# Kernel optimization log

Measured on AMD Instinct MI355X. Metric: run time of the kernel, lower is better.

Reference implementation:

```python
import jax, jax.numpy as jnp
import numpy as np

U, T, Q, K, H = 2048, 200, 4096, 16, 256
STD_THETA = 1.0
LMDA_THETA = 1.0 / STD_THETA**2


def setup_inputs() -> dict:
    key = jax.random.key(0)
    ks = jax.random.split(key, 10)
    q_id = jax.random.randint(ks[0], (U, T), 0, Q)
    kmap = jax.random.bernoulli(ks[1], 0.25, (Q, K))
    mask = jnp.ones((U, T), dtype=bool)
    resp = jnp.round(jax.random.uniform(ks[2], (U, T))).astype(jnp.float32)
    diff_mu = jax.random.normal(ks[3], (Q,), jnp.float32) * 0.5
    disc_mu = jax.random.normal(ks[4], (Q,), jnp.float32) * 0.5
    W1 = jax.random.normal(ks[5], (3, H), jnp.float32) * 0.3
    b1 = jnp.zeros((H,), jnp.float32)
    W2 = jax.random.normal(ks[6], (H, H), jnp.float32) * (1.0 / np.sqrt(H))
    b2 = jnp.zeros((H,), jnp.float32)
    W3 = jax.random.normal(ks[7], (H, 2), jnp.float32) * (1.0 / np.sqrt(H))
    b3 = jnp.zeros((2,), jnp.float32)
    return dict(mask=mask, q_id=q_id, kmap=kmap, resp=resp,
                diff_mu=diff_mu, disc_mu=disc_mu,
                W1=W1, b1=b1, W2=W2, b2=b2, W3=W3, b3=b3)


def _gelu(x):
    return jax.nn.gelu(x, approximate=False)  # torch nn.GELU default (erf)


def reference(mask, q_id, kmap, resp, diff_mu, disc_mu, W1, b1, W2, b2, W3, b3):
    # --- per-trial potentials (MLP input is identical across the KC axis) ---
    td = diff_mu[q_id]                       # (U,T)  diff gather
    ts = disc_mu[q_id]                       # (U,T)  disc gather
    inp = jnp.stack([td, ts, resp], axis=-1)  # (U,T,3)
    h = _gelu(inp @ W1 + b1)
    h = _gelu(h @ W2 + b2)
    poten = _gelu(h @ W3 + b3)               # (U,T,2)
    mu = poten[..., 0]                       # (U,T)
    logvar = jnp.maximum(poten[..., 1], 1e-8)
    lmda = jnp.exp(-logvar)                  # (U,T)

    m = jnp.moveaxis(kmap[q_id], 1, 0)       # (T,U,K) trial KC mask
    mu_T = mu.T                              # (T,U)
    lmda_T = lmda.T                          # (T,U)
    zUK = jnp.zeros((mu.shape[0], m.shape[-1]), mu.dtype)  # (U,K)

    # --- backward (Kalman-style) alpha/beta recursion; unmasked slots carry ---
    def bwd(carry, xs):
        alpha, beta = carry                  # (U,K) each
        l, mu_, msk = xs                     # (U,), (U,), (U,K)
        l = l[:, None]
        mu_ = mu_[:, None]
        a_new = (l + alpha * LMDA_THETA) / (LMDA_THETA + l + alpha * LMDA_THETA)
        b_new = (l * mu_ + a_new * l * beta) / (l + a_new * l)
        alpha2 = jnp.where(msk, a_new, alpha)
        beta2 = jnp.where(msk, b_new, beta)
        return (alpha2, beta2), alpha2

    _, alphas = jax.lax.scan(bwd, (zUK, zUK), (lmda_T, mu_T, m), reverse=True)
    # alpha_next[t] = alpha_{t+1} (zero past the end)
    alpha_next = jnp.concatenate([alphas[1:], zUK[None]], axis=0)  # (T,U,K)

    # --- forward posterior-mean ability update (deterministic mean path) ---
    def fwd(ability, xs):
        l, mu_, msk, a_nxt = xs
        l = l[:, None]
        mu_ = mu_[:, None]
        b_nxt = a_nxt  # replicates original: beta_next = alpha_lst[t+1]
        mu_tilde = (LMDA_THETA * ability + mu_ * l + a_nxt * LMDA_THETA * b_nxt) \
                   / (LMDA_THETA + l + a_nxt * LMDA_THETA)
        ab = jnp.where(msk, mu_tilde, ability)  # masked scatter / carry-through
        return ab, ab

    _, ab_tk = jax.lax.scan(fwd, zUK, (lmda_T, mu_T, m, alpha_next))  # (T,U,K)

    mf = m.astype(mu.dtype)
    trial_ability = ((ab_tk * mf).sum(-1) / jnp.maximum(mf.sum(-1), 1e-8)).T  # (U,T)
    return trial_ability
```

## Files before the change

kernel.cpp:

```cpp
#include <hip/hip_runtime.h>
#include <hip/hip_bf16.h>
#include <stdint.h>

#define U_DIM 2048
#define T_DIM 200
#define Q_DIM 4096
#define K_DIM 16
#define H_DIM 256
#define N_ROWS (Q_DIM * 2)

typedef float f4 __attribute__((ext_vector_type(4)));
typedef float f2 __attribute__((ext_vector_type(2)));

__device__ __forceinline__ float gelu_f(float x) {
    return 0.5f * x * (1.0f + erff(x * 0.70710678118654752440f));
}

__global__ __launch_bounds__(256) void pack_kmap_kernel(
    const uint8_t* __restrict__ kmap, uint32_t* __restrict__ mask_tab)
{
    __shared__ uint32_t sflag;
    int tid = threadIdx.x;
    if (tid < 64) {
        const uint32_t* kw = (const uint32_t*)kmap;
        uint32_t any = 0;
        #pragma unroll
        for (int i = 0; i < 16; ++i) any |= (kw[tid + 64 * i] > 1u) ? 1u : 0u;
        uint64_t b = __ballot(any != 0);
        if (tid == 0) sflag = (b != 0) ? 1u : 0u;
    }
    __syncthreads();
    int q = blockIdx.x * 256 + tid;
    uint32_t m = 0;
    if (sflag) {
        const uint32_t* p = (const uint32_t*)(kmap + (size_t)q * K_DIM);
        #pragma unroll
        for (int w = 0; w < 4; ++w) {
            uint32_t v = p[w];
            #pragma unroll
            for (int b = 0; b < 4; ++b)
                m |= (((v >> (8 * b)) & 0xffu) ? 1u : 0u) << (4 * w + b);
        }
    } else {
        const int* ki = (const int*)kmap + (size_t)q * K_DIM;
        #pragma unroll
        for (int k = 0; k < K_DIM; ++k)
            m |= (ki[k] ? 1u : 0u) << k;
    }
    mask_tab[q] = m;
}

__global__ __launch_bounds__(256) void mlp_table_kernel(
    const float* __restrict__ diff_mu, const float* __restrict__ disc_mu,
    const float* __restrict__ W1, const float* __restrict__ b1,
    const float* __restrict__ W2, const float* __restrict__ b2,
    const float* __restrict__ W3, const float* __restrict__ b3,
    float* __restrict__ mu_tab, float* __restrict__ lmda_tab)
{
    __shared__ float h1t[H_DIM][8];
    __shared__ float red[4][8][H_DIM];
    int tid  = threadIdx.x;
    int lane = tid & 63;
    int w    = tid >> 6;
    int row0 = blockIdx.x * 8;

    {
        int i = 64 * w + lane;
        float w1a = W1[0 * H_DIM + i], w1b = W1[1 * H_DIM + i],
              w1c = W1[2 * H_DIM + i], bi = b1[i];
        float hv[8];
        #pragma unroll
        for (int g = 0; g < 8; ++g) {
            int row = row0 + g;
            float td = diff_mu[row >> 1];
            float ts = disc_mu[row >> 1];
            float rr = (float)(row & 1);
            hv[g] = gelu_f(td * w1a + ts * w1b + rr * w1c + bi);
        }
        *(f4*)&h1t[i][0] = (f4){hv[0], hv[1], hv[2], hv[3]};
        *(f4*)&h1t[i][4] = (f4){hv[4], hv[5], hv[6], hv[7]};
    }
    __syncthreads();

    float acc[8][4];
    #pragma unroll
    for (int g = 0; g < 8; ++g) { acc[g][0] = acc[g][1] = acc[g][2] = acc[g][3] = 0.0f; }
    #pragma unroll 4
    for (int s = 0; s < 64; ++s) {
        int i = 64 * w + s;
        f4 wv = *(const f4*)&W2[i * H_DIM + 4 * lane];
        f4 hA = *(const f4*)&h1t[i][0];
        f4 hB = *(const f4*)&h1t[i][4];
        #pragma unroll
        for (int c = 0; c < 4; ++c) {
            acc[0][c] += hA[0] * wv[c];
            acc[1][c] += hA[1] * wv[c];
            acc[2][c] += hA[2] * wv[c];
            acc[3][c] += hA[3] * wv[c];
            acc[4][c] += hB[0] * wv[c];
            acc[5][c] += hB[1] * wv[c];
            acc[6][c] += hB[2] * wv[c];
            acc[7][c] += hB[3] * wv[c];
        }
    }
    #pragma unroll
    for (int g = 0; g < 8; ++g)
        *(f4*)&red[w][g][4 * lane] = (f4){acc[g][0], acc[g][1], acc[g][2], acc[g][3]};
    __syncthreads();

    if (tid < 128) {
        int w2 = tid >> 6;
        int l  = tid & 63;
        f4 bb2  = *(const f4*)&b2[4 * l];
        f4 w3lo = *(const f4*)&W3[8 * l];
        f4 w3hi = *(const f4*)&W3[8 * l + 4];
        float p0[4], p1[4];
        #pragma unroll
        for (int gg = 0; gg < 4; ++gg) {
            int g = 4 * w2 + gg;
            f4 s = bb2;
            #pragma unroll
            for (int ww = 0; ww < 4; ++ww) {
                f4 r = *(const f4*)&red[ww][g][4 * l];
                s[0] += r[0]; s[1] += r[1]; s[2] += r[2]; s[3] += r[3];
            }
            float h0 = gelu_f(s[0]), h1v = gelu_f(s[1]),
                  h2v = gelu_f(s[2]), h3v = gelu_f(s[3]);
            p0[gg] = h0 * w3lo[0] + h1v * w3lo[2] + h2v * w3hi[0] + h3v * w3hi[2];
            p1[gg] = h0 * w3lo[1] + h1v * w3lo[3] + h2v * w3hi[1] + h3v * w3hi[3];
        }
        #pragma unroll
        for (int gg = 0; gg < 4; ++gg) {
            #pragma unroll
            for (int off = 1; off < 64; off <<= 1) {
                p0[gg] += __shfl_xor(p0[gg], off);
                p1[gg] += __shfl_xor(p1[gg], off);
            }
        }
        if (l == 0) {
            float bb30 = b3[0], bb31 = b3[1];
            #pragma unroll
            for (int gg = 0; gg < 4; ++gg) {
                int row = row0 + 4 * w2 + gg;
                float mu = gelu_f(p0[gg] + bb30);
                float lv = gelu_f(p1[gg] + bb31);
                mu_tab[row]   = mu;
                lmda_tab[row] = expf(-fmaxf(lv, 1e-8f));
            }
        }
    }
}

__global__ __launch_bounds__(64) void scan_fused_kernel(
    const int* __restrict__ q_id, const float* __restrict__ resp,
    const float* __restrict__ mu_tab, const float* __restrict__ lmda_tab,
    const uint32_t* __restrict__ mask_tab, float* __restrict__ out)
{
    __shared__ float a_lds[64][201];
    __shared__ f2 la_lds[4][T_DIM];
    __shared__ uint16_t mk_lds[4][T_DIM];
    int tid = threadIdx.x;
    int u0 = blockIdx.x * 4;

    int   qv[13];
    float rv[13];
    #pragma unroll
    for (int p = 0; p < 13; ++p) {
        int idx = tid + 64 * p;
        if (idx < 4 * T_DIM) {
            int ul = idx / T_DIM, t = idx - ul * T_DIM;
            int g = (u0 + ul) * T_DIM + t;
            qv[p] = q_id[g];
            rv[p] = resp[g];
        }
    }
    #pragma unroll
    for (int p = 0; p < 13; ++p) {
        int idx = tid + 64 * p;
        if (idx < 4 * T_DIM) {
            int ul = idx / T_DIM, t = idx - ul * T_DIM;
            int ix = 2 * qv[p] + (rv[p] != 0.0f ? 1 : 0);
            float l  = lmda_tab[ix];
            float mu = mu_tab[ix];
            la_lds[ul][t] = (f2){1.0f + l, mu * l};
            mk_lds[ul][t] = (uint16_t)mask_tab[qv[p]];
        }
    }
    __syncthreads();

    int ul = tid >> 4, k = tid & 15;
    float* ap = a_lds[tid];
    const f2* la = la_lds[ul];
    const uint16_t* mk = mk_lds[ul];

    float alpha = 0.0f;
    float L1s0 = la[196][0], L1s1 = la[197][0], L1s2 = la[198][0], L1s3 = la[199][0];
    uint32_t ms0 = mk[196], ms1 = mk[197], ms2 = mk[198], ms3 = mk[199];
    for (int tb = 196; tb >= 0; tb -= 4) {
        int p3 = (tb >= 1) ? tb - 1 : 0;
        int p2 = (tb >= 2) ? tb - 2 : 0;
        int p1 = (tb >= 3) ? tb - 3 : 0;
        int p0 = (tb >= 4) ? tb - 4 : 0;
        { float L1 = L1s3; uint32_t m = ms3; L1s3 = la[p3][0]; ms3 = mk[p3];
          ap[tb + 3] = alpha;
          float an = 1.0f - __builtin_amdgcn_rcpf(L1 + alpha);
          alpha = ((m >> k) & 1) ? an : alpha; }
        { float L1 = L1s2; uint32_t m = ms2; L1s2 = la[p2][0]; ms2 = mk[p2];
          ap[tb + 2] = alpha;
          float an = 1.0f - __builtin_amdgcn_rcpf(L1 + alpha);
          alpha = ((m >> k) & 1) ? an : alpha; }
        { float L1 = L1s1; uint32_t m = ms1; L1s1 = la[p1][0]; ms1 = mk[p1];
          ap[tb + 1] = alpha;
          float an = 1.0f - __builtin_amdgcn_rcpf(L1 + alpha);
          alpha = ((m >> k) & 1) ? an : alpha; }
        { float L1 = L1s0; uint32_t m = ms0; L1s0 = la[p0][0]; ms0 = mk[p0];
          ap[tb + 0] = alpha;
          float an = 1.0f - __builtin_amdgcn_rcpf(L1 + alpha);
          alpha = ((m >> k) & 1) ? an : alpha; }
    }

    float ability = 0.0f;
    f2 lv0 = la[0], lv1 = la[1], lv2 = la[2], lv3 = la[3];
    uint32_t n0 = mk[0], n1 = mk[1], n2 = mk[2], n3 = mk[3];
    float av0 = ap[0], av1 = ap[1], av2 = ap[2], av3 = ap[3];
    for (int tb = 0; tb < 200; tb += 4) {
        int p0 = (tb + 4 < 200) ? tb + 4 : 199;
        int p1 = (tb + 5 < 200) ? tb + 5 : 199;
        int p2 = (tb + 6 < 200) ? tb + 6 : 199;
        int p3 = (tb + 7 < 200) ? tb + 7 : 199;
        { f2 v = lv0; uint32_t m = n0; float a = av0;
          lv0 = la[p0]; n0 = mk[p0]; av0 = ap[p0];
          float r = __builtin_amdgcn_rcpf(v[0] + a);
          float c1 = v[1] + a * a;
          float mt = (ability + c1) * r;
          bool msk = (m >> k) & 1;
          ability = msk ? mt : ability;
          ap[tb + 0] = msk ? ability : 0.0f; }
        { f2 v = lv1; uint32_t m = n1; float a = av1;
          lv1 = la[p1]; n1 = mk[p1]; av1 = ap[p1];
          float r = __builtin_amdgcn_rcpf(v[0] + a);
          float c1 = v[1] + a * a;
          float mt = (ability + c1) * r;
          bool msk = (m >> k) & 1;
          ability = msk ? mt : ability;
          ap[tb + 1] = msk ? ability : 0.0f; }
        { f2 v = lv2; uint32_t m = n2; float a = av2;
          lv2 = la[p2]; n2 = mk[p2]; av2 = ap[p2];
          float r = __builtin_amdgcn_rcpf(v[0] + a);
          float c1 = v[1] + a * a;
          float mt = (ability + c1) * r;
          bool msk = (m >> k) & 1;
          ability = msk ? mt : ability;
          ap[tb + 2] = msk ? ability : 0.0f; }
        { f2 v = lv3; uint32_t m = n3; float a = av3;
          lv3 = la[p3]; n3 = mk[p3]; av3 = ap[p3];
          float r = __builtin_amdgcn_rcpf(v[0] + a);
          float c1 = v[1] + a * a;
          float mt = (ability + c1) * r;
          bool msk = (m >> k) & 1;
          ability = msk ? mt : ability;
          ap[tb + 3] = msk ? ability : 0.0f; }
    }
    __syncthreads();

    #pragma unroll
    for (int p = 0; p < 13; ++p) {
        int idx = tid + 64 * p;
        if (idx < 4 * T_DIM) {
            int uo = idx / T_DIM, t = idx - uo * T_DIM;
            float s = 0.0f;
            #pragma unroll
            for (int kk = 0; kk < 16; ++kk) s += a_lds[uo * 16 + kk][t];
            float c = (float)__popc((unsigned)(mk_lds[uo][t] & 0xffffu));
            out[(u0 + uo) * T_DIM + t] = s * __builtin_amdgcn_rcpf(fmaxf(c, 1e-8f));
        }
    }
}

extern "C" void kernel_launch(void* const* d_in, const int* in_sizes, int n_in,
                              void* d_out, int out_size, void* d_ws, size_t ws_size,
                              hipStream_t stream) {
    const int*     q_id    = (const int*)d_in[1];
    const uint8_t* kmap    = (const uint8_t*)d_in[2];
    const float*   resp    = (const float*)d_in[3];
    const float*   diff_mu = (const float*)d_in[4];
    const float*   disc_mu = (const float*)d_in[5];
    const float*   W1      = (const float*)d_in[6];
    const float*   b1      = (const float*)d_in[7];
    const float*   W2      = (const float*)d_in[8];
    const float*   b2      = (const float*)d_in[9];
    const float*   W3      = (const float*)d_in[10];
    const float*   b3      = (const float*)d_in[11];
    float* out = (float*)d_out;

    char* w = (char*)d_ws;
    float* mu_tab      = (float*)w;      w += (size_t)N_ROWS * 4;
    float* lmda_tab    = (float*)w;      w += (size_t)N_ROWS * 4;
    uint32_t* mask_tab = (uint32_t*)w;   w += (size_t)Q_DIM * 4;

    hipLaunchKernelGGL(pack_kmap_kernel, dim3(Q_DIM / 256), dim3(256), 0, stream,
                       kmap, mask_tab);
    hipLaunchKernelGGL(mlp_table_kernel, dim3(N_ROWS / 8), dim3(256), 0, stream,
                       diff_mu, disc_mu, W1, b1, W2, b2, W3, b3, mu_tab, lmda_tab);
    hipLaunchKernelGGL(scan_fused_kernel, dim3(U_DIM / 4), dim3(64), 0, stream,
                       q_id, resp, mu_tab, lmda_tab, mask_tab, out);
}
```

Baseline: 121.9 us.

## Fuse kmap packing into MLP table kernel and double rows per block

Merges the kmap bit-packing kernel into the MLP table kernel, so the first 16 blocks also build the mask table, which removes one kernel launch. Each block now handles 16 table rows instead of 8, halving the grid and reusing each W2 load across twice as many rows. The cross-wave reduction runs in two phases over a reused shared buffer. This raises register pressure (64 accumulators per thread) and may lower occupancy.

```diff
diff --git a/kernel.cpp b/kernel.cpp
--- a/kernel.cpp
+++ b/kernel.cpp
@@ -16,136 +16,139 @@
     return 0.5f * x * (1.0f + erff(x * 0.70710678118654752440f));
 }
 
-__global__ __launch_bounds__(256) void pack_kmap_kernel(
-    const uint8_t* __restrict__ kmap, uint32_t* __restrict__ mask_tab)
-{
-    __shared__ uint32_t sflag;
-    int tid = threadIdx.x;
-    if (tid < 64) {
-        const uint32_t* kw = (const uint32_t*)kmap;
-        uint32_t any = 0;
-        #pragma unroll
-        for (int i = 0; i < 16; ++i) any |= (kw[tid + 64 * i] > 1u) ? 1u : 0u;
-        uint64_t b = __ballot(any != 0);
-        if (tid == 0) sflag = (b != 0) ? 1u : 0u;
-    }
-    __syncthreads();
-    int q = blockIdx.x * 256 + tid;
-    uint32_t m = 0;
-    if (sflag) {
-        const uint32_t* p = (const uint32_t*)(kmap + (size_t)q * K_DIM);
-        #pragma unroll
-        for (int w = 0; w < 4; ++w) {
-            uint32_t v = p[w];
-            #pragma unroll
-            for (int b = 0; b < 4; ++b)
-                m |= (((v >> (8 * b)) & 0xffu) ? 1u : 0u) << (4 * w + b);
-        }
-    } else {
-        const int* ki = (const int*)kmap + (size_t)q * K_DIM;
-        #pragma unroll
-        for (int k = 0; k < K_DIM; ++k)
-            m |= (ki[k] ? 1u : 0u) << k;
-    }
-    mask_tab[q] = m;
-}
-
-__global__ __launch_bounds__(256) void mlp_table_kernel(
+__global__ __launch_bounds__(256) void mlp_pack_kernel(
+    const uint8_t* __restrict__ kmap, uint32_t* __restrict__ mask_tab,
     const float* __restrict__ diff_mu, const float* __restrict__ disc_mu,
     const float* __restrict__ W1, const float* __restrict__ b1,
     const float* __restrict__ W2, const float* __restrict__ b2,
     const float* __restrict__ W3, const float* __restrict__ b3,
     float* __restrict__ mu_tab, float* __restrict__ lmda_tab)
 {
-    __shared__ float h1t[H_DIM][8];
-    __shared__ float red[4][8][H_DIM];
+    __shared__ float h1t[H_DIM][20];
+    __shared__ float red8[4][8][H_DIM];
+    __shared__ uint32_t sflag;
     int tid  = threadIdx.x;
-    int lane = tid & 63;
-    int w    = tid >> 6;
-    int row0 = blockIdx.x * 8;
+    int bid  = blockIdx.x;
+    int row0 = bid * 16;
+
+    if (bid < 16) {
+        if (tid < 64) {
+            const uint32_t* kw = (const uint32_t*)kmap;
+            uint32_t any = 0;
+            #pragma unroll
+            for (int i = 0; i < 16; ++i) any |= (kw[tid + 64 * i] > 1u) ? 1u : 0u;
+            uint64_t b = __ballot(any != 0);
+            if (tid == 0) sflag = (b != 0) ? 1u : 0u;
+        }
+        __syncthreads();
+        int q = bid * 256 + tid;
+        uint32_t m = 0;
+        if (sflag) {
+            const uint32_t* p = (const uint32_t*)(kmap + (size_t)q * K_DIM);
+            #pragma unroll
+            for (int w = 0; w < 4; ++w) {
+                uint32_t v = p[w];
+                #pragma unroll
+                for (int b = 0; b < 4; ++b)
+                    m |= (((v >> (8 * b)) & 0xffu) ? 1u : 0u) << (4 * w + b);
+            }
+        } else {
+            const int* ki = (const int*)kmap + (size_t)q * K_DIM;
+            #pragma unroll
+            for (int k = 0; k < K_DIM; ++k)
+                m |= (ki[k] ? 1u : 0u) << k;
+        }
+        mask_tab[q] = m;
+    }
 
     {
-        int i = 64 * w + lane;
-        float w1a = W1[0 * H_DIM + i], w1b = W1[1 * H_DIM + i],
-              w1c = W1[2 * H_DIM + i], bi = b1[i];
-        float hv[8];
+        int i = tid;
+        float w1a = W1[i], w1b = W1[H_DIM + i], w1c = W1[2 * H_DIM + i], bi = b1[i];
+        float hv[16];
         #pragma unroll
-        for (int g = 0; g < 8; ++g) {
+        for (int g = 0; g < 16; ++g) {
             int row = row0 + g;
             float td = diff_mu[row >> 1];
             float ts = disc_mu[row >> 1];
             float rr = (float)(row & 1);
             hv[g] = gelu_f(td * w1a + ts * w1b + rr * w1c + bi);
         }
-        *(f4*)&h1t[i][0] = (f4){hv[0], hv[1], hv[2], hv[3]};
-        *(f4*)&h1t[i][4] = (f4){hv[4], hv[5], hv[6], hv[7]};
+        *(f4*)&h1t[i][0]  = (f4){hv[0],  hv[1],  hv[2],  hv[3]};
+        *(f4*)&h1t[i][4]  = (f4){hv[4],  hv[5],  hv[6],  hv[7]};
+        *(f4*)&h1t[i][8]  = (f4){hv[8],  hv[9],  hv[10], hv[11]};
+        *(f4*)&h1t[i][12] = (f4){hv[12], hv[13], hv[14], hv[15]};
     }
     __syncthreads();
 
-    float acc[8][4];
-    #pragma unroll
-    for (int g = 0; g < 8; ++g) { acc[g][0] = acc[g][1] = acc[g][2] = acc[g][3] = 0.0f; }
+    int w = tid >> 6, l = tid & 63;
+    float acc[16][4];
+    #pragma unroll
+    for (int g = 0; g < 16; ++g)
+        acc[g][0] = acc[g][1] = acc[g][2] = acc[g][3] = 0.0f;
     #pragma unroll 4
     for (int s = 0; s < 64; ++s) {
-        int i = 64 * w + s;
-        f4 wv = *(const f4*)&W2[i * H_DIM + 4 * lane];
-        f4 hA = *(const f4*)&h1t[i][0];
-        f4 hB = *(const f4*)&h1t[i][4];
+        int i2 = 64 * w + s;
+        f4 wv = *(const f4*)&W2[i2 * H_DIM + 4 * l];
+        f4 hA = *(const f4*)&h1t[i2][0];
+        f4 hB = *(const f4*)&h1t[i2][4];
+        f4 hC = *(const f4*)&h1t[i2][8];
+        f4 hD = *(const f4*)&h1t[i2][12];
         #pragma unroll
         for (int c = 0; c < 4; ++c) {
-            acc[0][c] += hA[0] * wv[c];
-            acc[1][c] += hA[1] * wv[c];
-            acc[2][c] += hA[2] * wv[c];
-            acc[3][c] += hA[3] * wv[c];
-            acc[4][c] += hB[0] * wv[c];
-            acc[5][c] += hB[1] * wv[c];
-            acc[6][c] += hB[2] * wv[c];
-            acc[7][c] += hB[3] * wv[c];
-        }
-    }
-    #pragma unroll
-    for (int g = 0; g < 8; ++g)
-        *(f4*)&red[w][g][4 * lane] = (f4){acc[g][0], acc[g][1], acc[g][2], acc[g][3]};
-    __syncthreads();
-
-    if (tid < 128) {
-        int w2 = tid >> 6;
-        int l  = tid & 63;
-        f4 bb2  = *(const f4*)&b2[4 * l];
-        f4 w3lo = *(const f4*)&W3[8 * l];
-        f4 w3hi = *(const f4*)&W3[8 * l + 4];
-        float p0[4], p1[4];
+            acc[0][c]  += hA[0] * wv[c];
+            acc[1][c]  += hA[1] * wv[c];
+            acc[2][c]  += hA[2] * wv[c];
+            acc[3][c]  += hA[3] * wv[c];
+            acc[4][c]  += hB[0] * wv[c];
+            acc[5][c]  += hB[1] * wv[c];
+            acc[6][c]  += hB[2] * wv[c];
+            acc[7][c]  += hB[3] * wv[c];
+            acc[8][c]  += hC[0] * wv[c];
+            acc[9][c]  += hC[1] * wv[c];
+            acc[10][c] += hC[2] * wv[c];
+            acc[11][c] += hC[3] * wv[c];
+            acc[12][c] += hD[0] * wv[c];
+            acc[13][c] += hD[1] * wv[c];
+            acc[14][c] += hD[2] * wv[c];
+            acc[15][c] += hD[3] * wv[c];
+        }
+    }
+
+    f4 bb2  = *(const f4*)&b2[4 * l];
+    f4 w3lo = *(const f4*)&W3[8 * l];
+    f4 w3hi = *(const f4*)&W3[8 * l + 4];
+    float bb30 = b3[0], bb31 = b3[1];
+    #pragma unroll
+    for (int phase = 0; phase < 2; ++phase) {
+        int base = 8 * phase;
+        __syncthreads();
         #pragma unroll
-        for (int gg = 0; gg < 4; ++gg) {
-            int g = 4 * w2 + gg;
+        for (int g = 0; g < 8; ++g)
+            *(f4*)&red8[w][g][4 * l] =
+                (f4){acc[base + g][0], acc[base + g][1], acc[base + g][2], acc[base + g][3]};
+        __syncthreads();
+        #pragma unroll
+        for (int gg = 0; gg < 2; ++gg) {
+            int g = 2 * w + gg;
             f4 s = bb2;
             #pragma unroll
             for (int ww = 0; ww < 4; ++ww) {
-                f4 r = *(const f4*)&red[ww][g][4 * l];
+                f4 r = *(const f4*)&red8[ww][g][4 * l];
                 s[0] += r[0]; s[1] += r[1]; s[2] += r[2]; s[3] += r[3];
             }
             float h0 = gelu_f(s[0]), h1v = gelu_f(s[1]),
                   h2v = gelu_f(s[2]), h3v = gelu_f(s[3]);
-            p0[gg] = h0 * w3lo[0] + h1v * w3lo[2] + h2v * w3hi[0] + h3v * w3hi[2];
-            p1[gg] = h0 * w3lo[1] + h1v * w3lo[3] + h2v * w3hi[1] + h3v * w3hi[3];
-        }
-        #pragma unroll
-        for (int gg = 0; gg < 4; ++gg) {
+            float p0 = h0 * w3lo[0] + h1v * w3lo[2] + h2v * w3hi[0] + h3v * w3hi[2];
+            float p1 = h0 * w3lo[1] + h1v * w3lo[3] + h2v * w3hi[1] + h3v * w3hi[3];
             #pragma unroll
             for (int off = 1; off < 64; off <<= 1) {
-                p0[gg] += __shfl_xor(p0[gg], off);
-                p1[gg] += __shfl_xor(p1[gg], off);
+                p0 += __shfl_xor(p0, off);
+                p1 += __shfl_xor(p1, off);
             }
-        }
-        if (l == 0) {
-            float bb30 = b3[0], bb31 = b3[1];
-            #pragma unroll
-            for (int gg = 0; gg < 4; ++gg) {
-                int row = row0 + 4 * w2 + gg;
-                float mu = gelu_f(p0[gg] + bb30);
-                float lv = gelu_f(p1[gg] + bb31);
-                mu_tab[row]   = mu;
-                lmda_tab[row] = expf(-fmaxf(lv, 1e-8f));
+            if (l == 0) {
+                int row = row0 + base + g;
+                mu_tab[row]   = gelu_f(p0 + bb30);
+                lmda_tab[row] = expf(-fmaxf(gelu_f(p1 + bb31), 1e-8f));
             }
         }
     }
@@ -298,10 +301,9 @@
     float* lmda_tab    = (float*)w;      w += (size_t)N_ROWS * 4;
     uint32_t* mask_tab = (uint32_t*)w;   w += (size_t)Q_DIM * 4;
 
-    hipLaunchKernelGGL(pack_kmap_kernel, dim3(Q_DIM / 256), dim3(256), 0, stream,
-                       kmap, mask_tab);
-    hipLaunchKernelGGL(mlp_table_kernel, dim3(N_ROWS / 8), dim3(256), 0, stream,
-                       diff_mu, disc_mu, W1, b1, W2, b2, W3, b3, mu_tab, lmda_tab);
+    hipLaunchKernelGGL(mlp_pack_kernel, dim3(N_ROWS / 16), dim3(256), 0, stream,
+                       kmap, mask_tab, diff_mu, disc_mu,
+                       W1, b1, W2, b2, W3, b3, mu_tab, lmda_tab);
     hipLaunchKernelGGL(scan_fused_kernel, dim3(U_DIM / 4), dim3(64), 0, stream,
                        q_id, resp, mu_tab, lmda_tab, mask_tab, out);
 }
```

After: 119.7 us. Within noise of the previous version (-1.8%).
